# Kernel optimization log

Hardware: AMD Instinct MI355X
Metric: run time of the kernel (lower is better)

## Reference

```python
import jax, jax.numpy as jnp
import numpy as np

N = 6144
D_IN = 512
D_OUT = 512
DENSITY = 0.005


def setup_inputs() -> dict:
    key = jax.random.key(0)
    ks = jax.random.split(key, 12)
    x = jax.random.normal(ks[0], (N, D_IN), dtype=jnp.float32)
    adj_a = (jax.random.uniform(ks[1], (N, N)) < DENSITY).astype(jnp.float32)
    adj_b = (jax.random.uniform(ks[2], (N, N)) < DENSITY).astype(jnp.float32)
    # SparseAttention params (xavier-ish scale)
    W_sa = jax.random.normal(ks[3], (D_IN, D_OUT), dtype=jnp.float32) * (1.414 / np.sqrt(D_IN + D_OUT))
    a_sa = jax.random.normal(ks[4], (1, 2 * D_OUT), dtype=jnp.float32) * (1.414 / np.sqrt(1 + 2 * D_OUT))
    # GraphConvolution b params (uniform +-1/sqrt(out))
    stdv = 1.0 / np.sqrt(D_OUT)
    W_gcnb = jax.random.uniform(ks[5], (D_IN, D_OUT), minval=-stdv, maxval=stdv, dtype=jnp.float32)
    b_gcnb = jax.random.uniform(ks[6], (D_OUT,), minval=-stdv, maxval=stdv, dtype=jnp.float32)
    # gate Linear layers: Linear(2*D_IN, 1)
    s = 1.0 / np.sqrt(2 * D_IN)
    Wa = jax.random.uniform(ks[7], (1, 2 * D_IN), minval=-s, maxval=s, dtype=jnp.float32)
    ba = jax.random.uniform(ks[8], (1,), minval=-s, maxval=s, dtype=jnp.float32)
    Wb = jax.random.uniform(ks[9], (1, 2 * D_IN), minval=-s, maxval=s, dtype=jnp.float32)
    bb = jax.random.uniform(ks[10], (1,), minval=-s, maxval=s, dtype=jnp.float32)
    return {"x": x, "adj_a": adj_a, "adj_b": adj_b, "W_sa": W_sa, "a_sa": a_sa,
            "W_gcnb": W_gcnb, "b_gcnb": b_gcnb, "Wa": Wa, "ba": ba, "Wb": Wb, "bb": bb}


def reference(x, adj_a, adj_b, W_sa, a_sa, W_gcnb, b_gcnb, Wa, ba, Wb, bb):
    # type-level gates: sigmoid(Linear(cat[adj@x, x]))
    type_sum_a = adj_a @ x                      # [N, D_IN]
    type_sum_b = adj_b @ x
    attn_a = jax.nn.sigmoid(jnp.concatenate([type_sum_a, x], axis=1) @ Wa.T + ba)  # [N,1]
    attn_b = jax.nn.sigmoid(jnp.concatenate([type_sum_b, x], axis=1) @ Wb.T + bb)

    # SparseAttention over adj_a (edge pattern only)
    h = x @ W_sa                                # [N, D_OUT]
    Hd = h.shape[1]
    s_left = h @ a_sa[0, :Hd]                   # [N] contribution of source node i
    s_right = h @ a_sa[0, Hd:]                  # [N] contribution of target node j
    scores = s_left[:, None] + s_right[None, :]  # [N,N]
    e = jnp.where(adj_a != 0, jnp.exp(-jax.nn.leaky_relu(scores, 0.01)), 0.0)
    attn = e / (jnp.sum(e, axis=1, keepdims=True) + 1e-5)
    x_a = attn @ h                              # [N, D_OUT]

    # GCN branch over adj_b
    x_b = adj_b @ (x @ W_gcnb) + b_gcnb         # [N, D_OUT]

    return jax.nn.sigmoid(attn_a * x_a + attn_b * x_b)
```

## Files before the change

kernel.cpp:

```cpp
#include <hip/hip_runtime.h>
#include <math.h>

#define NN 6144
#define DD 512
#define CAP 128
#define WCAP 32

typedef __bf16 bf16_t;
typedef __bf16 bf16x8 __attribute__((ext_vector_type(8)));
typedef unsigned short u16x8 __attribute__((ext_vector_type(8)));
typedef float f32x4 __attribute__((ext_vector_type(4)));

__device__ __forceinline__ float bf2f(unsigned short u) {
    unsigned v = ((unsigned)u) << 16;
    return __builtin_bit_cast(float, v);
}
__device__ __forceinline__ unsigned short f2bf(float f) {
    unsigned u = __builtin_bit_cast(unsigned, f);
    u += 0x7fffu + ((u >> 16) & 1u);
    return (unsigned short)(u >> 16);
}
__device__ __forceinline__ float sigmoidf_(float z) { return 1.0f / (1.0f + expf(-z)); }

__global__ __launch_bounds__(256) void k_prep(const float* __restrict__ Wsa,
                                              const float* __restrict__ Wg,
                                              const float* __restrict__ x,
                                              const float* __restrict__ Wa,
                                              const float* __restrict__ Wb,
                                              unsigned short* __restrict__ wt,
                                              float* __restrict__ xal, float* __restrict__ xar,
                                              float* __restrict__ xbl, float* __restrict__ xbr) {
    __shared__ float s[64][65];
    int bid = blockIdx.x;
    if (bid < 128) {
        int n0 = (bid & 15) * 64;
        int k0 = (bid >> 4) * 64;
        int tx = threadIdx.x & 63, ty = threadIdx.x >> 6;
        const float* src = (n0 < 512) ? Wsa : Wg;
        int nn0 = n0 & 511;
#pragma unroll
        for (int kk = 0; kk < 64; kk += 4)
            s[kk + ty][tx] = src[(size_t)(k0 + kk + ty) * 512 + nn0 + tx];
        __syncthreads();
#pragma unroll
        for (int nn = 0; nn < 64; nn += 4)
            wt[(size_t)(n0 + nn + ty) * 512 + k0 + tx] = f2bf(s[tx][nn + ty]);
    } else {
        int wave = threadIdx.x >> 6, lane = threadIdx.x & 63;
        int row = (bid - 128) * 4 + wave;
        int k0 = lane * 8;
        const float* xr_ = x + (size_t)row * DD + k0;
        float4 v0 = *(const float4*)xr_;
        float4 v1 = *(const float4*)(xr_ + 4);
        float xv[8] = {v0.x, v0.y, v0.z, v0.w, v1.x, v1.y, v1.z, v1.w};
        float a0 = 0, a1 = 0, b0 = 0, b1 = 0;
#pragma unroll
        for (int j = 0; j < 8; j++) {
            a0 += xv[j] * Wa[k0 + j];
            a1 += xv[j] * Wa[512 + k0 + j];
            b0 += xv[j] * Wb[k0 + j];
            b1 += xv[j] * Wb[512 + k0 + j];
        }
#pragma unroll
        for (int off = 32; off; off >>= 1) {
            a0 += __shfl_down(a0, off); a1 += __shfl_down(a1, off);
            b0 += __shfl_down(b0, off); b1 += __shfl_down(b1, off);
        }
        if (lane == 0) { xal[row] = a0; xar[row] = a1; xbl[row] = b0; xbr[row] = b1; }
    }
}

__global__ __launch_bounds__(256) void k_big(const float* __restrict__ x,
                                             const bf16_t* __restrict__ wt,
                                             const float* __restrict__ adjA,
                                             const float* __restrict__ adjB,
                                             int* __restrict__ idxA, int* __restrict__ idxB,
                                             int* __restrict__ cntA, int* __restrict__ cntB,
                                             unsigned short* __restrict__ h,
                                             unsigned short* __restrict__ g) {
    int bid = blockIdx.x;
    int wave = threadIdx.x >> 6, lane = threadIdx.x & 63;
    if (bid < 2 * NN) {
        int which = bid >= NN;
        int row = which ? bid - NN : bid;
        const float* adj = which ? adjB : adjA;
        int* idx = (which ? idxB : idxA) + (size_t)row * CAP;

        const float4* arow = (const float4*)(adj + (size_t)row * NN);
        int base_i = wave * 384 + lane;
        float4 v[6];
#pragma unroll
        for (int j = 0; j < 6; j++) v[j] = arow[base_i + (size_t)j * 64];

        __shared__ int s_ent[4][WCAP];
        __shared__ int s_lc[4];
        unsigned long long below = (1ull << lane) - 1ull;
        int cnt = 0;
#pragma unroll
        for (int j = 0; j < 6; j++) {
            float f[4] = {v[j].x, v[j].y, v[j].z, v[j].w};
#pragma unroll
            for (int c = 0; c < 4; c++) {
                bool nz = (f[c] != 0.0f);
                unsigned long long m = __ballot(nz);
                if (nz) {
                    int pos = cnt + (int)__popcll(m & below);
                    if (pos < WCAP) s_ent[wave][pos] = (base_i + j * 64) * 4 + c;
                }
                cnt += (int)__popcll(m);
            }
        }
        if (cnt > WCAP) cnt = WCAP;
        if (lane == 0) s_lc[wave] = cnt;
        __syncthreads();
        int l0 = s_lc[0], l1 = s_lc[1], l2 = s_lc[2], l3 = s_lc[3];
        int total = l0 + l1 + l2 + l3;
        int t = threadIdx.x;
        if (t < total) {
            int w, o;
            if (t < l0) { w = 0; o = t; }
            else if (t < l0 + l1) { w = 1; o = t - l0; }
            else if (t < l0 + l1 + l2) { w = 2; o = t - l0 - l1; }
            else { w = 3; o = t - l0 - l1 - l2; }
            idx[t] = s_ent[w][o];
        }
        if (threadIdx.x == 0) (which ? cntB : cntA)[row] = total;
    } else {
        int tt = bid - 2 * NN;
        int row0 = (tt % (NN / 64)) * 64 + wave * 16;
        int col0 = (tt / (NN / 64)) * 64;
        int lr = lane & 15;
        int kg = (lane >> 4) * 8;

        f32x4 acc[4] = {{0,0,0,0},{0,0,0,0},{0,0,0,0},{0,0,0,0}};
        const float* ap = x + (size_t)(row0 + lr) * DD + kg;
        const bf16_t* bp = wt + (size_t)(col0 + lr) * DD + kg;

        for (int k0 = 0; k0 < DD; k0 += 32) {
            float4 a0 = *(const float4*)(ap + k0);
            float4 a1 = *(const float4*)(ap + k0 + 4);
            u16x8 au;
            au[0] = f2bf(a0.x); au[1] = f2bf(a0.y); au[2] = f2bf(a0.z); au[3] = f2bf(a0.w);
            au[4] = f2bf(a1.x); au[5] = f2bf(a1.y); au[6] = f2bf(a1.z); au[7] = f2bf(a1.w);
            bf16x8 a = __builtin_bit_cast(bf16x8, au);
#pragma unroll
            for (int n = 0; n < 4; n++) {
                bf16x8 b = *(const bf16x8*)(bp + (size_t)n * 16 * DD + k0);
                acc[n] = __builtin_amdgcn_mfma_f32_16x16x32_bf16(a, b, acc[n], 0, 0, 0);
            }
        }
        int dcol = lane & 15;
        int dr0 = (lane >> 4) * 4;
#pragma unroll
        for (int n = 0; n < 4; n++) {
            int col = col0 + n * 16 + dcol;
            unsigned short* dst = (col < 512) ? h : g;
            int cc = col & 511;
#pragma unroll
            for (int r = 0; r < 4; r++) {
                int m = row0 + dr0 + r;
                dst[(size_t)m * 512 + cc] = f2bf(acc[n][r]);
            }
        }
    }
}

__global__ __launch_bounds__(256) void k_gsl(const int* __restrict__ idxA, const int* __restrict__ cntA,
                                             const int* __restrict__ idxB, const int* __restrict__ cntB,
                                             const float* __restrict__ xal, const float* __restrict__ xar,
                                             const float* __restrict__ xbl, const float* __restrict__ xbr,
                                             const float* __restrict__ ba, const float* __restrict__ bb,
                                             const unsigned short* __restrict__ h,
                                             const float* __restrict__ a_sa,
                                             float* __restrict__ gateA, float* __restrict__ gateB,
                                             float* __restrict__ sl, float* __restrict__ sr) {
    int bid = blockIdx.x;
    int wave = threadIdx.x >> 6, lane = threadIdx.x & 63;
    if (bid < 3072) {
        int gw = bid * 4 + wave;
        int row = gw >> 1;
        int which = gw & 1;
        int cnt = (which ? cntB : cntA)[row];
        const int* idx = (which ? idxB : idxA) + (size_t)row * CAP;
        const float* xl = which ? xbl : xal;
        float s = 0.f;
        for (int t = lane; t < cnt; t += 64) s += xl[idx[t]];
#pragma unroll
        for (int off = 32; off; off >>= 1) s += __shfl_down(s, off);
        if (lane == 0) {
            float z = s + (which ? xbr : xar)[row] + (which ? bb : ba)[0];
            (which ? gateB : gateA)[row] = sigmoidf_(z);
        }
    } else {
        int row = (bid - 3072) * 4 + wave;
        int k0 = lane * 8;
        uint4 hv = *(const uint4*)(h + (size_t)row * DD + k0);
        unsigned u[4] = {hv.x, hv.y, hv.z, hv.w};
        float s0 = 0, s1 = 0;
#pragma unroll
        for (int j = 0; j < 4; j++) {
            float h0 = bf2f((unsigned short)(u[j] & 0xffff));
            float h1 = bf2f((unsigned short)(u[j] >> 16));
            s0 += h0 * a_sa[k0 + 2 * j] + h1 * a_sa[k0 + 2 * j + 1];
            s1 += h0 * a_sa[512 + k0 + 2 * j] + h1 * a_sa[512 + k0 + 2 * j + 1];
        }
#pragma unroll
        for (int off = 32; off; off >>= 1) { s0 += __shfl_down(s0, off); s1 += __shfl_down(s1, off); }
        if (lane == 0) { sl[row] = s0; sr[row] = s1; }
    }
}

__global__ __launch_bounds__(256) void k_final(
    const int* __restrict__ idxA, const int* __restrict__ cntA,
    const int* __restrict__ idxB, const int* __restrict__ cntB,
    const unsigned short* __restrict__ h, const unsigned short* __restrict__ g,
    const float* __restrict__ sl, const float* __restrict__ sr,
    const float* __restrict__ gateA, const float* __restrict__ gateB,
    const float* __restrict__ bias, float* __restrict__ out) {
    int i = blockIdx.x;
    int tid = threadIdx.x;
    __shared__ float w[CAP];
    __shared__ int ja[CAP], jb[CAP];
    __shared__ float s_denom;

    int cA = cntA[i], cB = cntB[i];
    if (tid < cA) {
        int j = idxA[(size_t)i * CAP + tid];
        ja[tid] = j;
        float s = sl[i] + sr[j];
        float lrelu = s > 0.f ? s : 0.01f * s;
        w[tid] = expf(-lrelu);
    }
    if (tid < cB) jb[tid] = idxB[(size_t)i * CAP + tid];
    __syncthreads();

    if (tid < 64) {
        float p = 0.f;
        for (int t = tid; t < cA; t += 64) p += w[t];
#pragma unroll
        for (int off = 32; off; off >>= 1) p += __shfl_down(p, off);
        if (tid == 0) s_denom = p;
    }
    __syncthreads();
    float inv = 1.f / (s_denom + 1e-5f);
    if (tid < cA) w[tid] *= inv;
    __syncthreads();

    float ga = gateA[i], gb = gateB[i];
    int d0 = tid * 2;
    float a0 = 0, a1 = 0, b0 = 0, b1 = 0;
#pragma unroll 4
    for (int t = 0; t < cA; t++) {
        unsigned hv = *(const unsigned*)(h + (size_t)ja[t] * 512 + d0);
        float wt_ = w[t];
        a0 += wt_ * bf2f((unsigned short)(hv & 0xffff));
        a1 += wt_ * bf2f((unsigned short)(hv >> 16));
    }
#pragma unroll 4
    for (int t = 0; t < cB; t++) {
        unsigned gv = *(const unsigned*)(g + (size_t)jb[t] * 512 + d0);
        b0 += bf2f((unsigned short)(gv & 0xffff));
        b1 += bf2f((unsigned short)(gv >> 16));
    }
    float z0 = ga * a0 + gb * (b0 + bias[d0]);
    float z1 = ga * a1 + gb * (b1 + bias[d0 + 1]);
    out[(size_t)i * 512 + d0]     = sigmoidf_(z0);
    out[(size_t)i * 512 + d0 + 1] = sigmoidf_(z1);
}

extern "C" void kernel_launch(void* const* d_in, const int* in_sizes, int n_in,
                              void* d_out, int out_size, void* d_ws, size_t ws_size,
                              hipStream_t stream) {
    const float* x    = (const float*)d_in[0];
    const float* adjA = (const float*)d_in[1];
    const float* adjB = (const float*)d_in[2];
    const float* Wsa  = (const float*)d_in[3];
    const float* a_sa = (const float*)d_in[4];
    const float* Wg   = (const float*)d_in[5];
    const float* bg   = (const float*)d_in[6];
    const float* Wa   = (const float*)d_in[7];
    const float* ba   = (const float*)d_in[8];
    const float* Wb   = (const float*)d_in[9];
    const float* bb   = (const float*)d_in[10];
    float* out = (float*)d_out;

    char* ws = (char*)d_ws;
    size_t off = 0;
    auto alloc = [&](size_t bytes) -> void* {
        void* p = ws + off;
        off += (bytes + 255) & ~(size_t)255;
        return p;
    };
    unsigned short* wt = (unsigned short*)alloc((size_t)1024 * DD * 2);
    unsigned short* h  = (unsigned short*)alloc((size_t)NN * DD * 2);
    unsigned short* g  = (unsigned short*)alloc((size_t)NN * DD * 2);
    int* idxA = (int*)alloc((size_t)NN * CAP * 4);
    int* idxB = (int*)alloc((size_t)NN * CAP * 4);
    int* cntA = (int*)alloc((size_t)NN * 4);
    int* cntB = (int*)alloc((size_t)NN * 4);
    float* xal = (float*)alloc((size_t)NN * 4);
    float* xar = (float*)alloc((size_t)NN * 4);
    float* xbl = (float*)alloc((size_t)NN * 4);
    float* xbr = (float*)alloc((size_t)NN * 4);
    float* gateA = (float*)alloc((size_t)NN * 4);
    float* gateB = (float*)alloc((size_t)NN * 4);
    float* sl = (float*)alloc((size_t)NN * 4);
    float* sr = (float*)alloc((size_t)NN * 4);

    k_prep<<<128 + NN / 4, 256, 0, stream>>>(Wsa, Wg, x, Wa, Wb, wt, xal, xar, xbl, xbr);
    k_big<<<2 * NN + (NN / 64) * (1024 / 64), 256, 0, stream>>>(
        x, (const bf16_t*)wt, adjA, adjB, idxA, idxB, cntA, cntB, h, g);
    k_gsl<<<3072 + NN / 4, 256, 0, stream>>>(idxA, cntA, idxB, cntB, xal, xar, xbl, xbr,
                                             ba, bb, h, a_sa, gateA, gateB, sl, sr);
    k_final<<<NN, 256, 0, stream>>>(idxA, cntA, idxB, cntB, h, g, sl, sr, gateA, gateB, bg, out);
}
```

Baseline: 172.3 us.

## Scan adjacency rows per wave, interleave with GEMM tiles, fold gates into final kernel

The adjacency compaction now gives each wave a whole row. Each lane loads 24 float4 values, builds bitmasks and uses a wave prefix scan to write indices, which removes the per-element ballots, the shared-memory staging and the block barrier. Compaction blocks and GEMM tiles are interleaved in one grid so the memory-bound scan and the MFMA work overlap. The gate sums and sigmoid move into the final kernel, and the softmax normalisation is applied at the end, removing a kernel stage, the gate buffers and one barrier. The old per-wave cap of 32 entries is replaced by a single cap of 128 per row.

```diff
diff --git a/kernel.cpp b/kernel.cpp
--- a/kernel.cpp
+++ b/kernel.cpp
@@ -4,7 +4,6 @@
 #define NN 6144
 #define DD 512
 #define CAP 128
-#define WCAP 32
 
 typedef __bf16 bf16_t;
 typedef __bf16 bf16x8 __attribute__((ext_vector_type(8)));
@@ -70,63 +69,65 @@
     }
 }
 
-__global__ __launch_bounds__(256) void k_big(const float* __restrict__ x,
-                                             const bf16_t* __restrict__ wt,
-                                             const float* __restrict__ adjA,
-                                             const float* __restrict__ adjB,
-                                             int* __restrict__ idxA, int* __restrict__ idxB,
-                                             int* __restrict__ cntA, int* __restrict__ cntB,
-                                             unsigned short* __restrict__ h,
-                                             unsigned short* __restrict__ g) {
+__global__ __launch_bounds__(256) void k_fused(const float* __restrict__ x,
+                                               const bf16_t* __restrict__ wt,
+                                               const float* __restrict__ adjA,
+                                               const float* __restrict__ adjB,
+                                               int* __restrict__ idxA, int* __restrict__ idxB,
+                                               int* __restrict__ cntA, int* __restrict__ cntB,
+                                               unsigned short* __restrict__ h,
+                                               unsigned short* __restrict__ g) {
     int bid = blockIdx.x;
     int wave = threadIdx.x >> 6, lane = threadIdx.x & 63;
-    if (bid < 2 * NN) {
-        int which = bid >= NN;
-        int row = which ? bid - NN : bid;
+    int grp = bid % 3;
+    if (grp < 2) {
+        int sid = (bid / 3) * 2 + grp;
+        int row = sid * 4 + wave;
+        int which = row >= NN;
+        int r = which ? row - NN : row;
         const float* adj = which ? adjB : adjA;
-        int* idx = (which ? idxB : idxA) + (size_t)row * CAP;
-
-        const float4* arow = (const float4*)(adj + (size_t)row * NN);
-        int base_i = wave * 384 + lane;
-        float4 v[6];
-#pragma unroll
-        for (int j = 0; j < 6; j++) v[j] = arow[base_i + (size_t)j * 64];
-
-        __shared__ int s_ent[4][WCAP];
-        __shared__ int s_lc[4];
-        unsigned long long below = (1ull << lane) - 1ull;
-        int cnt = 0;
-#pragma unroll
-        for (int j = 0; j < 6; j++) {
-            float f[4] = {v[j].x, v[j].y, v[j].z, v[j].w};
-#pragma unroll
-            for (int c = 0; c < 4; c++) {
-                bool nz = (f[c] != 0.0f);
-                unsigned long long m = __ballot(nz);
-                if (nz) {
-                    int pos = cnt + (int)__popcll(m & below);
-                    if (pos < WCAP) s_ent[wave][pos] = (base_i + j * 64) * 4 + c;
-                }
-                cnt += (int)__popcll(m);
+        int* idx = (which ? idxB : idxA) + (size_t)r * CAP;
+        int* cnt = which ? cntB : cntA;
+
+        const float4* arow = (const float4*)(adj + (size_t)r * NN) + lane;
+        float4 v[24];
+#pragma unroll
+        for (int j = 0; j < 24; j++) v[j] = arow[j * 64];
+
+        unsigned m[3] = {0, 0, 0};
+#pragma unroll
+        for (int j = 0; j < 24; j++) {
+            unsigned w_ = (j >> 3);
+            unsigned sh = (j & 7) * 4;
+            m[w_] |= (v[j].x != 0.f ? 1u : 0u) << sh;
+            m[w_] |= (v[j].y != 0.f ? 1u : 0u) << (sh + 1);
+            m[w_] |= (v[j].z != 0.f ? 1u : 0u) << (sh + 2);
+            m[w_] |= (v[j].w != 0.f ? 1u : 0u) << (sh + 3);
+        }
+        int c = __popc(m[0]) + __popc(m[1]) + __popc(m[2]);
+        int p = c;
+#pragma unroll
+        for (int off = 1; off < 64; off <<= 1) {
+            int t = __shfl_up(p, off);
+            if (lane >= off) p += t;
+        }
+        int pos = p - c;
+        int total = __shfl(p, 63);
+#pragma unroll
+        for (int w_ = 0; w_ < 3; w_++) {
+            unsigned mm = m[w_];
+            while (mm) {
+                int b = __ffs(mm) - 1;
+                mm &= mm - 1;
+                int e = w_ * 32 + b;
+                int col = (e >> 2) * 256 + lane * 4 + (e & 3);
+                if (pos < CAP) idx[pos] = col;
+                pos++;
             }
         }
-        if (cnt > WCAP) cnt = WCAP;
-        if (lane == 0) s_lc[wave] = cnt;
-        __syncthreads();
-        int l0 = s_lc[0], l1 = s_lc[1], l2 = s_lc[2], l3 = s_lc[3];
-        int total = l0 + l1 + l2 + l3;
-        int t = threadIdx.x;
-        if (t < total) {
-            int w, o;
-            if (t < l0) { w = 0; o = t; }
-            else if (t < l0 + l1) { w = 1; o = t - l0; }
-            else if (t < l0 + l1 + l2) { w = 2; o = t - l0 - l1; }
-            else { w = 3; o = t - l0 - l1 - l2; }
-            idx[t] = s_ent[w][o];
-        }
-        if (threadIdx.x == 0) (which ? cntB : cntA)[row] = total;
+        if (lane == 0) cnt[r] = total > CAP ? CAP : total;
     } else {
-        int tt = bid - 2 * NN;
+        int tt = bid / 3;
         int row0 = (tt % (NN / 64)) * 64 + wave * 16;
         int col0 = (tt / (NN / 64)) * 64;
         int lr = lane & 15;
@@ -158,56 +159,32 @@
             int cc = col & 511;
 #pragma unroll
             for (int r = 0; r < 4; r++) {
-                int m = row0 + dr0 + r;
-                dst[(size_t)m * 512 + cc] = f2bf(acc[n][r]);
+                int mr = row0 + dr0 + r;
+                dst[(size_t)mr * 512 + cc] = f2bf(acc[n][r]);
             }
         }
     }
 }
 
-__global__ __launch_bounds__(256) void k_gsl(const int* __restrict__ idxA, const int* __restrict__ cntA,
-                                             const int* __restrict__ idxB, const int* __restrict__ cntB,
-                                             const float* __restrict__ xal, const float* __restrict__ xar,
-                                             const float* __restrict__ xbl, const float* __restrict__ xbr,
-                                             const float* __restrict__ ba, const float* __restrict__ bb,
-                                             const unsigned short* __restrict__ h,
+__global__ __launch_bounds__(256) void k_slr(const unsigned short* __restrict__ h,
                                              const float* __restrict__ a_sa,
-                                             float* __restrict__ gateA, float* __restrict__ gateB,
                                              float* __restrict__ sl, float* __restrict__ sr) {
-    int bid = blockIdx.x;
     int wave = threadIdx.x >> 6, lane = threadIdx.x & 63;
-    if (bid < 3072) {
-        int gw = bid * 4 + wave;
-        int row = gw >> 1;
-        int which = gw & 1;
-        int cnt = (which ? cntB : cntA)[row];
-        const int* idx = (which ? idxB : idxA) + (size_t)row * CAP;
-        const float* xl = which ? xbl : xal;
-        float s = 0.f;
-        for (int t = lane; t < cnt; t += 64) s += xl[idx[t]];
-#pragma unroll
-        for (int off = 32; off; off >>= 1) s += __shfl_down(s, off);
-        if (lane == 0) {
-            float z = s + (which ? xbr : xar)[row] + (which ? bb : ba)[0];
-            (which ? gateB : gateA)[row] = sigmoidf_(z);
-        }
-    } else {
-        int row = (bid - 3072) * 4 + wave;
-        int k0 = lane * 8;
-        uint4 hv = *(const uint4*)(h + (size_t)row * DD + k0);
-        unsigned u[4] = {hv.x, hv.y, hv.z, hv.w};
-        float s0 = 0, s1 = 0;
-#pragma unroll
-        for (int j = 0; j < 4; j++) {
-            float h0 = bf2f((unsigned short)(u[j] & 0xffff));
-            float h1 = bf2f((unsigned short)(u[j] >> 16));
-            s0 += h0 * a_sa[k0 + 2 * j] + h1 * a_sa[k0 + 2 * j + 1];
-            s1 += h0 * a_sa[512 + k0 + 2 * j] + h1 * a_sa[512 + k0 + 2 * j + 1];
-        }
-#pragma unroll
-        for (int off = 32; off; off >>= 1) { s0 += __shfl_down(s0, off); s1 += __shfl_down(s1, off); }
-        if (lane == 0) { sl[row] = s0; sr[row] = s1; }
-    }
+    int row = blockIdx.x * 4 + wave;
+    int k0 = lane * 8;
+    uint4 hv = *(const uint4*)(h + (size_t)row * DD + k0);
+    unsigned u[4] = {hv.x, hv.y, hv.z, hv.w};
+    float s0 = 0, s1 = 0;
+#pragma unroll
+    for (int j = 0; j < 4; j++) {
+        float h0 = bf2f((unsigned short)(u[j] & 0xffff));
+        float h1 = bf2f((unsigned short)(u[j] >> 16));
+        s0 += h0 * a_sa[k0 + 2 * j] + h1 * a_sa[k0 + 2 * j + 1];
+        s1 += h0 * a_sa[512 + k0 + 2 * j] + h1 * a_sa[512 + k0 + 2 * j + 1];
+    }
+#pragma unroll
+    for (int off = 32; off; off >>= 1) { s0 += __shfl_down(s0, off); s1 += __shfl_down(s1, off); }
+    if (lane == 0) { sl[row] = s0; sr[row] = s1; }
 }
 
 __global__ __launch_bounds__(256) void k_final(
@@ -215,13 +192,15 @@
     const int* __restrict__ idxB, const int* __restrict__ cntB,
     const unsigned short* __restrict__ h, const unsigned short* __restrict__ g,
     const float* __restrict__ sl, const float* __restrict__ sr,
-    const float* __restrict__ gateA, const float* __restrict__ gateB,
+    const float* __restrict__ xal, const float* __restrict__ xar,
+    const float* __restrict__ xbl, const float* __restrict__ xbr,
+    const float* __restrict__ ba, const float* __restrict__ bb,
     const float* __restrict__ bias, float* __restrict__ out) {
     int i = blockIdx.x;
     int tid = threadIdx.x;
     __shared__ float w[CAP];
     __shared__ int ja[CAP], jb[CAP];
-    __shared__ float s_denom;
+    __shared__ float s_denom, s_ga, s_gb;
 
     int cA = cntA[i], cB = cntB[i];
     if (tid < cA) {
@@ -235,18 +214,25 @@
     __syncthreads();
 
     if (tid < 64) {
-        float p = 0.f;
-        for (int t = tid; t < cA; t += 64) p += w[t];
-#pragma unroll
-        for (int off = 32; off; off >>= 1) p += __shfl_down(p, off);
-        if (tid == 0) s_denom = p;
+        float p = 0.f, gasum = 0.f, gbsum = 0.f;
+        for (int t = tid; t < cA; t += 64) { p += w[t]; gasum += xal[ja[t]]; }
+        for (int t = tid; t < cB; t += 64) gbsum += xbl[jb[t]];
+#pragma unroll
+        for (int off = 32; off; off >>= 1) {
+            p += __shfl_down(p, off);
+            gasum += __shfl_down(gasum, off);
+            gbsum += __shfl_down(gbsum, off);
+        }
+        if (tid == 0) {
+            s_denom = p;
+            s_ga = sigmoidf_(gasum + xar[i] + ba[0]);
+            s_gb = sigmoidf_(gbsum + xbr[i] + bb[0]);
+        }
     }
     __syncthreads();
     float inv = 1.f / (s_denom + 1e-5f);
-    if (tid < cA) w[tid] *= inv;
-    __syncthreads();
-
-    float ga = gateA[i], gb = gateB[i];
+    float ga = s_ga, gb = s_gb;
+
     int d0 = tid * 2;
     float a0 = 0, a1 = 0, b0 = 0, b1 = 0;
 #pragma unroll 4
@@ -262,8 +248,8 @@
         b0 += bf2f((unsigned short)(gv & 0xffff));
         b1 += bf2f((unsigned short)(gv >> 16));
     }
-    float z0 = ga * a0 + gb * (b0 + bias[d0]);
-    float z1 = ga * a1 + gb * (b1 + bias[d0 + 1]);
+    float z0 = ga * (a0 * inv) + gb * (b0 + bias[d0]);
+    float z1 = ga * (a1 * inv) + gb * (b1 + bias[d0 + 1]);
     out[(size_t)i * 512 + d0]     = sigmoidf_(z0);
     out[(size_t)i * 512 + d0 + 1] = sigmoidf_(z1);
 }
@@ -302,15 +288,13 @@
     float* xar = (float*)alloc((size_t)NN * 4);
     float* xbl = (float*)alloc((size_t)NN * 4);
     float* xbr = (float*)alloc((size_t)NN * 4);
-    float* gateA = (float*)alloc((size_t)NN * 4);
-    float* gateB = (float*)alloc((size_t)NN * 4);
     float* sl = (float*)alloc((size_t)NN * 4);
     float* sr = (float*)alloc((size_t)NN * 4);
 
     k_prep<<<128 + NN / 4, 256, 0, stream>>>(Wsa, Wg, x, Wa, Wb, wt, xal, xar, xbl, xbr);
-    k_big<<<2 * NN + (NN / 64) * (1024 / 64), 256, 0, stream>>>(
-        x, (const bf16_t*)wt, adjA, adjB, idxA, idxB, cntA, cntB, h, g);
-    k_gsl<<<3072 + NN / 4, 256, 0, stream>>>(idxA, cntA, idxB, cntB, xal, xar, xbl, xbr,
-                                             ba, bb, h, a_sa, gateA, gateB, sl, sr);
-    k_final<<<NN, 256, 0, stream>>>(idxA, cntA, idxB, cntB, h, g, sl, sr, gateA, gateB, bg, out);
-}
+    k_fused<<<4608, 256, 0, stream>>>(x, (const bf16_t*)wt, adjA, adjB,
+                                      idxA, idxB, cntA, cntB, h, g);
+    k_slr<<<NN / 4, 256, 0, stream>>>(h, a_sa, sl, sr);
+    k_final<<<NN, 256, 0, stream>>>(idxA, cntA, idxB, cntB, h, g, sl, sr,
+                                    xal, xar, xbl, xbr, ba, bb, bg, out);
+}
```

Measured after the change: 168.4 us. 1.02x faster.
